# Kernel tuning notes

Measured on AMD Instinct MI355X. Metric: run time of the kernel, lower is better.

The kernel has to match this reference:

```python
import jax, jax.numpy as jnp
import numpy as np

N, E, IN_DIM, B = 20000, 320000, 256, 64
H0, C0 = 4, 128   # layer0: concat -> 512
H1, C1 = 4, 64    # layer1: mean over heads -> 64
NEG_SLOPE = 0.2
BN_EPS = 1e-5


def _p(key, shape, scale=0.05):
    return scale * jax.random.normal(key, shape, dtype=jnp.float32)


def setup_inputs() -> dict:
    key = jax.random.key(0)
    ks = jax.random.split(key, 32)
    inp = {
        'x': jax.random.normal(ks[0], (N, IN_DIM), dtype=jnp.float32),
        'edge_index': jax.random.randint(ks[1], (2, E), 0, N, dtype=jnp.int64),
        'edge_attr': jax.random.uniform(ks[2], (E, 1), dtype=jnp.float32),
        'batch': jnp.sort(jax.random.randint(ks[3], (N,), 0, B, dtype=jnp.int64)),
        # GATv2 layer 0: in=256 -> H0*C0=512 (concat)
        'g0_wl': _p(ks[4], (IN_DIM, H0 * C0)),
        'g0_wr': _p(ks[5], (IN_DIM, H0 * C0)),
        'g0_we': _p(ks[6], (1, H0 * C0)),
        'g0_att': _p(ks[7], (H0, C0)),
        'g0_bias': jnp.zeros((H0 * C0,), jnp.float32),
        'bn0_g': jnp.ones((H0 * C0,), jnp.float32),
        'bn0_b': jnp.zeros((H0 * C0,), jnp.float32),
        # GATv2 layer 1: in=512 -> C1=64 (mean over heads)
        'g1_wl': _p(ks[8], (H0 * C0, H1 * C1)),
        'g1_wr': _p(ks[9], (H0 * C0, H1 * C1)),
        'g1_we': _p(ks[10], (1, H1 * C1)),
        'g1_att': _p(ks[11], (H1, C1)),
        'g1_bias': jnp.zeros((C1,), jnp.float32),
        'bn1_g': jnp.ones((C1,), jnp.float32),
        'bn1_b': jnp.zeros((C1,), jnp.float32),
        # classifier: 64 -> 256 -> 128 -> 2 with BN+ELU
        'c_w1': _p(ks[12], (C1, 256)), 'c_b1': jnp.zeros((256,), jnp.float32),
        'cbn1_g': jnp.ones((256,), jnp.float32), 'cbn1_b': jnp.zeros((256,), jnp.float32),
        'c_w2': _p(ks[13], (256, 128)), 'c_b2': jnp.zeros((128,), jnp.float32),
        'cbn2_g': jnp.ones((128,), jnp.float32), 'cbn2_b': jnp.zeros((128,), jnp.float32),
        'c_w3': _p(ks[14], (128, 2)), 'c_b3': jnp.zeros((2,), jnp.float32),
    }
    return inp


def gatv2_conv(x, src, dst, edge_attr, wl, wr, we, att, bias, heads, ch, concat):
    """GATv2Conv: gather -> LeakyReLU score -> segment softmax over dst -> scatter-add."""
    n = x.shape[0]
    xl = (x @ wl).reshape(n, heads, ch)
    xr = (x @ wr).reshape(n, heads, ch)
    xe = (edge_attr @ we).reshape(-1, heads, ch)
    m = xl[src] + xr[dst] + xe                                  # [E,H,C]
    e = jnp.einsum('ehc,hc->eh', jax.nn.leaky_relu(m, NEG_SLOPE), att)
    e_max = jax.ops.segment_max(e, dst, num_segments=n)          # [N,H]
    e_exp = jnp.exp(e - e_max[dst])
    denom = jax.ops.segment_sum(e_exp, dst, num_segments=n)
    alpha = e_exp / (denom[dst] + 1e-16)                         # [E,H]
    out = jax.ops.segment_sum(alpha[:, :, None] * xl[src], dst, num_segments=n)
    out = out.reshape(n, heads * ch) if concat else out.mean(axis=1)
    return out + bias


def batchnorm(x, g, b):
    mu = x.mean(axis=0)
    var = x.var(axis=0)
    return (x - mu) * jax.lax.rsqrt(var + BN_EPS) * g + b


def reference(x, edge_index, edge_attr, batch,
              g0_wl, g0_wr, g0_we, g0_att, g0_bias, bn0_g, bn0_b,
              g1_wl, g1_wr, g1_we, g1_att, g1_bias, bn1_g, bn1_b,
              c_w1, c_b1, cbn1_g, cbn1_b, c_w2, c_b2, cbn2_g, cbn2_b, c_w3, c_b3):
    src, dst = edge_index[0], edge_index[1]
    # layer 0 (concat=True)
    h = gatv2_conv(x, src, dst, edge_attr, g0_wl, g0_wr, g0_we, g0_att, g0_bias, H0, C0, True)
    h = jax.nn.elu(batchnorm(h, bn0_g, bn0_b))  # dropout = identity (eval)
    # layer 1 (concat=False -> mean over heads)
    h = gatv2_conv(h, src, dst, edge_attr, g1_wl, g1_wr, g1_we, g1_att, g1_bias, H1, C1, False)
    h = jax.nn.elu(batchnorm(h, bn1_g, bn1_b))
    # global mean pool per graph
    sums = jax.ops.segment_sum(h, batch, num_segments=B)
    cnts = jax.ops.segment_sum(jnp.ones((h.shape[0], 1), h.dtype), batch, num_segments=B)
    emb = sums / jnp.maximum(cnts, 1.0)                          # [B, 64]
    # classifier MLP
    z = jax.nn.elu(batchnorm(emb @ c_w1 + c_b1, cbn1_g, cbn1_b))
    z = jax.nn.elu(batchnorm(z @ c_w2 + c_b2, cbn2_g, cbn2_b))
    logits = z @ c_w3 + c_b3                                     # [B, 2]
    return logits, emb
```

## Files before the change

### kernel.cpp

```cpp
#include <hip/hip_runtime.h>
#include <cmath>

#define Nn 20000
#define Ee 320000
#define Bb 64

typedef unsigned short u16;
typedef __bf16 bf16x8 __attribute__((ext_vector_type(8)));
typedef float f32x4 __attribute__((ext_vector_type(4)));

static const size_t OUT0 = 0;
static const size_t XL0B = 10240000;
static const size_t XR0B = 15360000;
static const size_t H0B  = 20480000;
static const size_t XB   = 25600000;
static const size_t WTS  = 28160000;
static const size_t OUT1 = 28422144;
static const size_t CSRI = 30982144;
static const size_t SMALL= 31342272;
static const size_t BN0S = SMALL;
static const size_t BN1S = BN0S + 1024;
static const size_t ZCNT = 1152;
static const size_t EMB  = BN1S + 128;
static const size_t Z1C  = EMB + 4096;
static const size_t Z2C  = Z1C + 16384;

__device__ __forceinline__ float lrelu(float x){ return x > 0.f ? x : 0.2f * x; }
__device__ __forceinline__ float elu(float x){ return x > 0.f ? x : expm1f(x); }
__device__ __forceinline__ u16 fbf(float f){
  unsigned u = __float_as_uint(f);
  return (u16)((u + 0x7fffu + ((u >> 16) & 1u)) >> 16);
}
__device__ __forceinline__ float blo(unsigned u){ return __uint_as_float(u << 16); }
__device__ __forceinline__ float bhi(unsigned u){ return __uint_as_float(u & 0xffff0000u); }

__global__ __launch_bounds__(256) void mega_setup(
    const float* __restrict__ x, u16* __restrict__ xb,
    const float* __restrict__ W0, const float* __restrict__ W1,
    const float* __restrict__ W2, const float* __restrict__ W3,
    u16* __restrict__ WTo,
    const int* __restrict__ ei, int* __restrict__ cursor,
    const int* __restrict__ batch, int* __restrict__ goffs){
  int b = blockIdx.x;
  if (b < 5000){
    int i = b * 256 + threadIdx.x;
    float4 v = ((const float4*)x)[i];
    ushort4 o; o.x = fbf(v.x); o.y = fbf(v.y); o.z = fbf(v.z); o.w = fbf(v.w);
    ((ushort4*)xb)[i] = o;
  } else if (b < 7048){
    int bb2 = b - 5000;
    int which = bb2 >> 9;
    const float* W = (which == 0) ? W0 : (which == 1) ? W1 : (which == 2) ? W2 : W3;
    int K = (which < 2) ? 256 : 512;
    int N = (which < 2) ? 512 : 256;
    int i = (bb2 & 511) * 256 + threadIdx.x;
    int n = i / K, k = i - n * K;
    WTo[which * 131072 + i] = fbf(W[k * N + n]);
  } else if (b < 8298){
    int e = (b - 7048) * 256 + threadIdx.x;
    atomicAdd(&cursor[ei[Ee + e]], 1);
  } else {
    int i = (b - 8298) * 256 + threadIdx.x;
    if (i >= Nn) return;
    int b1 = batch[i];
    int b0 = (i == 0) ? -1 : batch[i - 1];
    for (int g = b0 + 1; g <= b1; g++) goffs[g] = i;
    if (i == Nn - 1)
      for (int g = b1 + 1; g <= Bb; g++) goffs[g] = Nn;
  }
}

__global__ __launch_bounds__(256) void gemm_lds(const u16* __restrict__ A,
    const u16* __restrict__ WTa, const u16* __restrict__ WTb,
    u16* __restrict__ Oa, u16* __restrict__ Ob, int M, int K, int Nc){
  const u16* WT = blockIdx.z ? WTb : WTa;
  u16* O = blockIdx.z ? Ob : Oa;
  __shared__ u16 As[128 * 32];
  __shared__ u16 Bs[128 * 32];
  int tid = threadIdx.x;
  int m0 = blockIdx.y * 128, n0 = blockIdx.x * 128;
  int lane = tid & 63, w = tid >> 6;
  int wr = (w >> 1) * 64, wc = (w & 1) * 64;
  int l16 = lane & 15, kq = lane >> 4;
  int sr0 = w * 16 + (lane >> 2);
  int sr1 = 64 + sr0;
  int sc8 = (lane & 3) * 8;
  const u16* ga0 = &A[(size_t)(m0 + sr0) * K + sc8];
  const u16* ga1 = &A[(size_t)(m0 + sr1) * K + sc8];
  const u16* gb0 = &WT[(size_t)(n0 + sr0) * K + sc8];
  const u16* gb1 = &WT[(size_t)(n0 + sr1) * K + sc8];
  u16* lA0 = &As[w * 512];
  u16* lA1 = &As[2048 + w * 512];
  u16* lB0 = &Bs[w * 512];
  u16* lB1 = &Bs[2048 + w * 512];
  f32x4 acc[4][4] = {};
  for (int kt = 0; kt < K; kt += 32){
    __builtin_amdgcn_global_load_lds(
        (const __attribute__((address_space(1))) unsigned int*)(ga0 + kt),
        (__attribute__((address_space(3))) unsigned int*)lA0, 16, 0, 0);
    __builtin_amdgcn_global_load_lds(
        (const __attribute__((address_space(1))) unsigned int*)(ga1 + kt),
        (__attribute__((address_space(3))) unsigned int*)lA1, 16, 0, 0);
    __builtin_amdgcn_global_load_lds(
        (const __attribute__((address_space(1))) unsigned int*)(gb0 + kt),
        (__attribute__((address_space(3))) unsigned int*)lB0, 16, 0, 0);
    __builtin_amdgcn_global_load_lds(
        (const __attribute__((address_space(1))) unsigned int*)(gb1 + kt),
        (__attribute__((address_space(3))) unsigned int*)lB1, 16, 0, 0);
    __syncthreads();
    bf16x8 af[4], bfr[4];
    #pragma unroll
    for (int i = 0; i < 4; i++){
      af[i]  = *(bf16x8*)&As[(wr + i * 16 + l16) * 32 + kq * 8];
      bfr[i] = *(bf16x8*)&Bs[(wc + i * 16 + l16) * 32 + kq * 8];
    }
    #pragma unroll
    for (int i = 0; i < 4; i++)
      #pragma unroll
      for (int j = 0; j < 4; j++)
        acc[i][j] = __builtin_amdgcn_mfma_f32_16x16x32_bf16(af[i], bfr[j], acc[i][j], 0, 0, 0);
    __syncthreads();
  }
  #pragma unroll
  for (int i = 0; i < 4; i++){
    #pragma unroll
    for (int rg = 0; rg < 4; rg++){
      int row = m0 + wr + i * 16 + kq * 4 + rg;
      if (row < M){
        #pragma unroll
        for (int j = 0; j < 4; j++){
          int col = n0 + wc + j * 16 + l16;
          O[(size_t)row * Nc + col] = fbf(acc[i][j][rg]);
        }
      }
    }
  }
}

__global__ __launch_bounds__(1024) void csr_scan(int* __restrict__ offs,
                                                 int* __restrict__ cursor){
  __shared__ int part[1024];
  int t = threadIdx.x;
  int base = t * 20;
  int loc[20];
  int s = 0;
  #pragma unroll
  for (int i = 0; i < 20; i++){
    int idx = base + i;
    int v = (idx < Nn) ? cursor[idx] : 0;
    loc[i] = s; s += v;
  }
  part[t] = s;
  __syncthreads();
  for (int off = 1; off < 1024; off <<= 1){
    int v = 0;
    if (t >= off) v = part[t - off];
    __syncthreads();
    if (t >= off) part[t] += v;
    __syncthreads();
  }
  int pre = (t == 0) ? 0 : part[t - 1];
  #pragma unroll
  for (int i = 0; i < 20; i++){
    int idx = base + i;
    if (idx < Nn){ offs[idx] = pre + loc[i]; cursor[idx] = pre + loc[i]; }
  }
  if (t == 1023) offs[Nn] = part[1023];
}

__global__ __launch_bounds__(256) void csr_fill(const int* __restrict__ ei,
    int* __restrict__ cursor, int* __restrict__ eidx){
  int e = blockIdx.x * 256 + threadIdx.x;
  if (e < Ee){
    int d = ei[Ee + e];
    int p = atomicAdd(&cursor[d], 1);
    eidx[p] = e;
  }
}

__global__ __launch_bounds__(256) void fused_l0(const u16* __restrict__ xl,
    const u16* __restrict__ xr, const float* __restrict__ ea,
    const float* __restrict__ we, const float* __restrict__ att,
    const int* __restrict__ ei, const int* __restrict__ offs,
    const int* __restrict__ eidx, float* __restrict__ out){
  int n = blockIdx.x * 4 + (threadIdx.x >> 6);
  int lane = threadIdx.x & 63;
  int s = offs[n], e = offs[n + 1];
  int c = lane << 3;
  uint4 ru = *(const uint4*)&xr[(size_t)n * 512 + c];
  float r0=blo(ru.x), r1=bhi(ru.x), r2=blo(ru.y), r3=bhi(ru.y),
        r4=blo(ru.z), r5=bhi(ru.z), r6=blo(ru.w), r7=bhi(ru.w);
  float4 w0 = *(const float4*)&we[c],  w1 = *(const float4*)&we[c + 4];
  float4 t0 = *(const float4*)&att[c], t1 = *(const float4*)&att[c + 4];
  float d = 0.f;
  float a0=0.f,a1=0.f,a2=0.f,a3=0.f,a4=0.f,a5=0.f,a6=0.f,a7=0.f;
  int i = s;
  for (; i + 2 <= e; i += 2){
    int eA = eidx[i], eB = eidx[i + 1];
    int sA = ei[eA], sB = ei[eB];
    float avA = ea[eA], avB = ea[eB];
    uint4 luA = *(const uint4*)&xl[(size_t)sA * 512 + c];
    uint4 luB = *(const uint4*)&xl[(size_t)sB * 512 + c];
    float xA0=blo(luA.x), xA1=bhi(luA.x), xA2=blo(luA.y), xA3=bhi(luA.y),
          xA4=blo(luA.z), xA5=bhi(luA.z), xA6=blo(luA.w), xA7=bhi(luA.w);
    float xB0=blo(luB.x), xB1=bhi(luB.x), xB2=blo(luB.y), xB3=bhi(luB.y),
          xB4=blo(luB.z), xB5=bhi(luB.z), xB6=blo(luB.w), xB7=bhi(luB.w);
    float pA = lrelu(xA0+r0+avA*w0.x)*t0.x + lrelu(xA1+r1+avA*w0.y)*t0.y
             + lrelu(xA2+r2+avA*w0.z)*t0.z + lrelu(xA3+r3+avA*w0.w)*t0.w
             + lrelu(xA4+r4+avA*w1.x)*t1.x + lrelu(xA5+r5+avA*w1.y)*t1.y
             + lrelu(xA6+r6+avA*w1.z)*t1.z + lrelu(xA7+r7+avA*w1.w)*t1.w;
    float pB = lrelu(xB0+r0+avB*w0.x)*t0.x + lrelu(xB1+r1+avB*w0.y)*t0.y
             + lrelu(xB2+r2+avB*w0.z)*t0.z + lrelu(xB3+r3+avB*w0.w)*t0.w
             + lrelu(xB4+r4+avB*w1.x)*t1.x + lrelu(xB5+r5+avB*w1.y)*t1.y
             + lrelu(xB6+r6+avB*w1.z)*t1.z + lrelu(xB7+r7+avB*w1.w)*t1.w;
    pA += __shfl_xor(pA, 8); pB += __shfl_xor(pB, 8);
    pA += __shfl_xor(pA, 4); pB += __shfl_xor(pB, 4);
    pA += __shfl_xor(pA, 2); pB += __shfl_xor(pB, 2);
    pA += __shfl_xor(pA, 1); pB += __shfl_xor(pB, 1);
    float eeA = __expf(pA), eeB = __expf(pB);
    d += eeA + eeB;
    a0 += eeA*xA0 + eeB*xB0; a1 += eeA*xA1 + eeB*xB1;
    a2 += eeA*xA2 + eeB*xB2; a3 += eeA*xA3 + eeB*xB3;
    a4 += eeA*xA4 + eeB*xB4; a5 += eeA*xA5 + eeB*xB5;
    a6 += eeA*xA6 + eeB*xB6; a7 += eeA*xA7 + eeB*xB7;
  }
  if (i < e){
    int eA = eidx[i];
    int sA = ei[eA];
    float avA = ea[eA];
    uint4 luA = *(const uint4*)&xl[(size_t)sA * 512 + c];
    float x0=blo(luA.x), x1=bhi(luA.x), x2=blo(luA.y), x3=bhi(luA.y),
          x4=blo(luA.z), x5=bhi(luA.z), x6=blo(luA.w), x7=bhi(luA.w);
    float p = lrelu(x0+r0+avA*w0.x)*t0.x + lrelu(x1+r1+avA*w0.y)*t0.y
            + lrelu(x2+r2+avA*w0.z)*t0.z + lrelu(x3+r3+avA*w0.w)*t0.w
            + lrelu(x4+r4+avA*w1.x)*t1.x + lrelu(x5+r5+avA*w1.y)*t1.y
            + lrelu(x6+r6+avA*w1.z)*t1.z + lrelu(x7+r7+avA*w1.w)*t1.w;
    p += __shfl_xor(p, 8); p += __shfl_xor(p, 4);
    p += __shfl_xor(p, 2); p += __shfl_xor(p, 1);
    float ee = __expf(p);
    d += ee;
    a0 += ee*x0; a1 += ee*x1; a2 += ee*x2; a3 += ee*x3;
    a4 += ee*x4; a5 += ee*x5; a6 += ee*x6; a7 += ee*x7;
  }
  float inv = 1.f / (d + 1e-16f);
  float4* op = (float4*)&out[(size_t)n * 512 + c];
  op[0] = make_float4(a0*inv, a1*inv, a2*inv, a3*inv);
  op[1] = make_float4(a4*inv, a5*inv, a6*inv, a7*inv);
}

__global__ __launch_bounds__(256) void fused_l1(const u16* __restrict__ xl,
    const u16* __restrict__ xr, const float* __restrict__ ea,
    const float* __restrict__ we, const float* __restrict__ att,
    const int* __restrict__ ei, const int* __restrict__ offs,
    const int* __restrict__ eidx, float* __restrict__ out){
  int n = blockIdx.x * 4 + (threadIdx.x >> 6);
  int lane = threadIdx.x & 63;
  int s = offs[n], e = offs[n + 1];
  int c = lane << 2;
  uint2 ru = *(const uint2*)&xr[(size_t)n * 256 + c];
  float r0=blo(ru.x), r1=bhi(ru.x), r2=blo(ru.y), r3=bhi(ru.y);
  float4 w  = *(const float4*)&we[c];
  float4 tt = *(const float4*)&att[c];
  float d = 0.f;
  float a0=0.f,a1=0.f,a2=0.f,a3=0.f;
  int i = s;
  for (; i + 2 <= e; i += 2){
    int eA = eidx[i], eB = eidx[i + 1];
    int sA = ei[eA], sB = ei[eB];
    float avA = ea[eA], avB = ea[eB];
    uint2 luA = *(const uint2*)&xl[(size_t)sA * 256 + c];
    uint2 luB = *(const uint2*)&xl[(size_t)sB * 256 + c];
    float xA0=blo(luA.x), xA1=bhi(luA.x), xA2=blo(luA.y), xA3=bhi(luA.y);
    float xB0=blo(luB.x), xB1=bhi(luB.x), xB2=blo(luB.y), xB3=bhi(luB.y);
    float pA = lrelu(xA0+r0+avA*w.x)*tt.x + lrelu(xA1+r1+avA*w.y)*tt.y
             + lrelu(xA2+r2+avA*w.z)*tt.z + lrelu(xA3+r3+avA*w.w)*tt.w;
    float pB = lrelu(xB0+r0+avB*w.x)*tt.x + lrelu(xB1+r1+avB*w.y)*tt.y
             + lrelu(xB2+r2+avB*w.z)*tt.z + lrelu(xB3+r3+avB*w.w)*tt.w;
    pA += __shfl_xor(pA, 8); pB += __shfl_xor(pB, 8);
    pA += __shfl_xor(pA, 4); pB += __shfl_xor(pB, 4);
    pA += __shfl_xor(pA, 2); pB += __shfl_xor(pB, 2);
    pA += __shfl_xor(pA, 1); pB += __shfl_xor(pB, 1);
    float eeA = __expf(pA), eeB = __expf(pB);
    d += eeA + eeB;
    a0 += eeA*xA0 + eeB*xB0; a1 += eeA*xA1 + eeB*xB1;
    a2 += eeA*xA2 + eeB*xB2; a3 += eeA*xA3 + eeB*xB3;
  }
  if (i < e){
    int eA = eidx[i];
    int sA = ei[eA];
    float avA = ea[eA];
    uint2 lu = *(const uint2*)&xl[(size_t)sA * 256 + c];
    float x0=blo(lu.x), x1=bhi(lu.x), x2=blo(lu.y), x3=bhi(lu.y);
    float p = lrelu(x0+r0+avA*w.x)*tt.x + lrelu(x1+r1+avA*w.y)*tt.y
            + lrelu(x2+r2+avA*w.z)*tt.z + lrelu(x3+r3+avA*w.w)*tt.w;
    p += __shfl_xor(p, 8); p += __shfl_xor(p, 4);
    p += __shfl_xor(p, 2); p += __shfl_xor(p, 1);
    float ee = __expf(p);
    d += ee;
    a0 += ee*x0; a1 += ee*x1; a2 += ee*x2; a3 += ee*x3;
  }
  float inv = 0.25f / (d + 1e-16f);
  float v0 = a0*inv, v1 = a1*inv, v2 = a2*inv, v3 = a3*inv;
  v0 += __shfl_xor(v0, 16); v0 += __shfl_xor(v0, 32);
  v1 += __shfl_xor(v1, 16); v1 += __shfl_xor(v1, 32);
  v2 += __shfl_xor(v2, 16); v2 += __shfl_xor(v2, 32);
  v3 += __shfl_xor(v3, 16); v3 += __shfl_xor(v3, 32);
  if (lane < 16)
    *(float4*)&out[(size_t)n * 64 + lane * 4] = make_float4(v0, v1, v2, v3);
}

__global__ void bn_reduce(const float* __restrict__ X, float* __restrict__ stats,
                          int Nr, int C, int rpb){
  int tid = threadIdx.x;
  int c = tid % C, sub = tid / C, step = blockDim.x / C;
  float s = 0.f, s2 = 0.f;
  int rend = min((int)((blockIdx.x + 1) * rpb), Nr);
  for (int r = blockIdx.x * rpb + sub; r < rend; r += step){
    float v = X[(size_t)r * C + c];
    s += v; s2 += v * v;
  }
  atomicAdd(&stats[c], s);
  atomicAdd(&stats[C + c], s2);
}

__global__ __launch_bounds__(256) void bn_apply_bf(const float* __restrict__ X,
    const float* __restrict__ stats, const float* __restrict__ g,
    const float* __restrict__ b, u16* __restrict__ Xb, int total, int C, float invN){
  int idx = blockIdx.x * 256 + threadIdx.x;
  if (idx >= total) return;
  int c = idx % C;
  float mean = stats[c] * invN;
  float var = stats[C + c] * invN - mean * mean;
  float inv = rsqrtf(var + 1e-5f);
  float v = (X[idx] - mean) * inv * g[c] + b[c];
  Xb[idx] = fbf(elu(v));
}

__global__ __launch_bounds__(256) void bn_apply(float* __restrict__ X,
    const float* __restrict__ stats, const float* __restrict__ g,
    const float* __restrict__ b, int total, int C, float invN){
  int idx = blockIdx.x * 256 + threadIdx.x;
  if (idx >= total) return;
  int c = idx % C;
  float mean = stats[c] * invN;
  float var = stats[C + c] * invN - mean * mean;
  float inv = rsqrtf(var + 1e-5f);
  float v = (X[idx] - mean) * inv * g[c] + b[c];
  X[idx] = elu(v);
}

__global__ __launch_bounds__(256) void pool_graph(const float* __restrict__ h1,
    const int* __restrict__ goffs, float* __restrict__ emb, float* __restrict__ out_emb){
  int b = blockIdx.x;
  int s = goffs[b], e = goffs[b + 1];
  int c = threadIdx.x & 63, sub = threadIdx.x >> 6;
  float acc = 0.f;
  for (int n = s + sub; n < e; n += 4) acc += h1[(size_t)n * 64 + c];
  __shared__ float red[4][64];
  red[sub][c] = acc;
  __syncthreads();
  if (sub == 0){
    float v = red[0][c] + red[1][c] + red[2][c] + red[3][c];
    v /= fmaxf((float)(e - s), 1.0f);
    emb[b * 64 + c] = v;
    out_emb[b * 64 + c] = v;
  }
}

__global__ __launch_bounds__(256) void mlp1_par(const float* __restrict__ emb,
    const float* __restrict__ W1, const float* __restrict__ b1,
    const float* __restrict__ g, const float* __restrict__ bb,
    float* __restrict__ z1){
  int t = threadIdx.x;
  int jj = t & 15, rg = t >> 4;
  int j = blockIdx.x * 16 + jj;
  float acc[4];
  float bias = b1[j];
  #pragma unroll
  for (int r = 0; r < 4; r++) acc[r] = bias;
  for (int k = 0; k < 64; k++){
    float w = W1[k * 256 + j];
    #pragma unroll
    for (int r = 0; r < 4; r++) acc[r] += emb[(rg * 4 + r) * 64 + k] * w;
  }
  __shared__ float ssum[16][16], ssq[16][16];
  float s = 0.f, s2 = 0.f;
  #pragma unroll
  for (int r = 0; r < 4; r++){ s += acc[r]; s2 += acc[r] * acc[r]; }
  ssum[rg][jj] = s; ssq[rg][jj] = s2;
  __syncthreads();
  float S = 0.f, S2 = 0.f;
  #pragma unroll
  for (int q = 0; q < 16; q++){ S += ssum[q][jj]; S2 += ssq[q][jj]; }
  float mean = S * (1.f / 64.f);
  float var = S2 * (1.f / 64.f) - mean * mean;
  float inv = rsqrtf(var + 1e-5f);
  float sc = g[j] * inv, sh = bb[j] - mean * sc;
  #pragma unroll
  for (int r = 0; r < 4; r++)
    z1[(rg * 4 + r) * 256 + j] = elu(acc[r] * sc + sh);
}

__global__ __launch_bounds__(256) void mlp2_fast(const float* __restrict__ z1,
    const float* __restrict__ W2, const float* __restrict__ b2,
    const float* __restrict__ g, const float* __restrict__ bb,
    float* __restrict__ z2){
  __shared__ float z1T[128 * 68];
  __shared__ float w2s[256 * 17];
  __shared__ float ssum[16][16], ssq[16][16];
  int t = threadIdx.x;
  int jj = t & 15, rg = t >> 4;
  int j = blockIdx.x * 16 + jj;
  {
    int j0 = blockIdx.x * 16;
    #pragma unroll
    for (int q = 0; q < 4; q++){
      float4 v = *(const float4*)&W2[t * 128 + j0 + q * 4];
      w2s[t * 17 + q * 4 + 0] = v.x; w2s[t * 17 + q * 4 + 1] = v.y;
      w2s[t * 17 + q * 4 + 2] = v.z; w2s[t * 17 + q * 4 + 3] = v.w;
    }
  }
  float acc[4];
  float bias = b2[j];
  #pragma unroll
  for (int r = 0; r < 4; r++) acc[r] = bias;
  for (int kk = 0; kk < 2; kk++){
    #pragma unroll
    for (int p = 0; p < 8; p++){
      int idx4 = p * 256 + t;
      int row = idx4 >> 5, kq = idx4 & 31;
      float4 v = *(const float4*)&z1[row * 256 + kk * 128 + kq * 4];
      z1T[(kq * 4 + 0) * 68 + row] = v.x;
      z1T[(kq * 4 + 1) * 68 + row] = v.y;
      z1T[(kq * 4 + 2) * 68 + row] = v.z;
      z1T[(kq * 4 + 3) * 68 + row] = v.w;
    }
    __syncthreads();
    for (int k = 0; k < 128; k++){
      float w = w2s[(kk * 128 + k) * 17 + jj];
      float4 zv = *(const float4*)&z1T[k * 68 + rg * 4];
      acc[0] += zv.x * w; acc[1] += zv.y * w;
      acc[2] += zv.z * w; acc[3] += zv.w * w;
    }
    __syncthreads();
  }
  float s = 0.f, s2 = 0.f;
  #pragma unroll
  for (int r = 0; r < 4; r++){ s += acc[r]; s2 += acc[r] * acc[r]; }
  ssum[rg][jj] = s; ssq[rg][jj] = s2;
  __syncthreads();
  float S = 0.f, S2 = 0.f;
  #pragma unroll
  for (int q = 0; q < 16; q++){ S += ssum[q][jj]; S2 += ssq[q][jj]; }
  float mean = S * (1.f / 64.f);
  float var = S2 * (1.f / 64.f) - mean * mean;
  float inv = rsqrtf(var + 1e-5f);
  float sc = g[j] * inv, sh = bb[j] - mean * sc;
  #pragma unroll
  for (int r = 0; r < 4; r++)
    z2[(rg * 4 + r) * 128 + j] = elu(acc[r] * sc + sh);
}

__global__ __launch_bounds__(256) void mlp3_fast(const float* __restrict__ z2,
    const float* __restrict__ W3, const float* __restrict__ b3, float* __restrict__ out){
  __shared__ float z2s[64 * 132];
  __shared__ float w3s[256];
  int t = threadIdx.x;
  #pragma unroll
  for (int p = 0; p < 8; p++){
    int idx4 = p * 256 + t;
    int row = idx4 >> 5, kq = idx4 & 31;
    float4 v = *(const float4*)&z2[row * 128 + kq * 4];
    z2s[row * 132 + kq * 4 + 0] = v.x;
    z2s[row * 132 + kq * 4 + 1] = v.y;
    z2s[row * 132 + kq * 4 + 2] = v.z;
    z2s[row * 132 + kq * 4 + 3] = v.w;
  }
  if (t < 64){
    float4 v = ((const float4*)W3)[t];
    w3s[t * 4 + 0] = v.x; w3s[t * 4 + 1] = v.y;
    w3s[t * 4 + 2] = v.z; w3s[t * 4 + 3] = v.w;
  }
  __syncthreads();
  if (t < 128){
    int row = t >> 1, o = t & 1;
    float acc = b3[o];
    for (int k = 0; k < 128; k++)
      acc += z2s[row * 132 + k] * w3s[k * 2 + o];
    out[row * 2 + o] = acc;
  }
}

extern "C" void kernel_launch(void* const* d_in, const int* in_sizes, int n_in,
                              void* d_out, int out_size, void* d_ws, size_t ws_size,
                              hipStream_t stream){
  const float* x      = (const float*)d_in[0];
  const int*   ei     = (const int*)d_in[1];
  const float* ea     = (const float*)d_in[2];
  const int*   batch  = (const int*)d_in[3];
  const float* g0_wl  = (const float*)d_in[4];
  const float* g0_wr  = (const float*)d_in[5];
  const float* g0_we  = (const float*)d_in[6];
  const float* g0_att = (const float*)d_in[7];
  const float* bn0_g  = (const float*)d_in[9];
  const float* bn0_b  = (const float*)d_in[10];
  const float* g1_wl  = (const float*)d_in[11];
  const float* g1_wr  = (const float*)d_in[12];
  const float* g1_we  = (const float*)d_in[13];
  const float* g1_att = (const float*)d_in[14];
  const float* bn1_g  = (const float*)d_in[16];
  const float* bn1_b  = (const float*)d_in[17];
  const float* c_w1   = (const float*)d_in[18];
  const float* c_b1   = (const float*)d_in[19];
  const float* cbn1_g = (const float*)d_in[20];
  const float* cbn1_b = (const float*)d_in[21];
  const float* c_w2   = (const float*)d_in[22];
  const float* c_b2   = (const float*)d_in[23];
  const float* cbn2_g = (const float*)d_in[24];
  const float* cbn2_b = (const float*)d_in[25];
  const float* c_w3   = (const float*)d_in[26];
  const float* c_b3   = (const float*)d_in[27];
  float* out = (float*)d_out;
  float* ws = (float*)d_ws;

  u16* xb   = (u16*)(ws + XB);
  u16* xl0b = (u16*)(ws + XL0B);
  u16* xr0b = (u16*)(ws + XR0B);
  u16* h0b  = (u16*)(ws + H0B);
  u16* wt0a = (u16*)(ws + WTS);
  u16* wt0b = wt0a + 131072;
  u16* wt1a = wt0a + 262144;
  u16* wt1b = wt0a + 393216;
  int* offs   = (int*)(ws + CSRI);
  int* cursor = offs + (Nn + 1);
  int* eidx   = cursor + Nn;
  int* goffs  = eidx + Ee;

  hipMemsetAsync(cursor, 0, Nn * sizeof(int), stream);
  hipMemsetAsync(ws + SMALL, 0, ZCNT * sizeof(float), stream);

  mega_setup<<<8377, 256, 0, stream>>>(x, xb, g0_wl, g0_wr, g1_wl, g1_wr, wt0a,
                                       ei, cursor, batch, goffs);
  csr_scan<<<1, 1024, 0, stream>>>(offs, cursor);
  csr_fill<<<(Ee + 255) / 256, 256, 0, stream>>>(ei, cursor, eidx);

  gemm_lds<<<dim3(4, 157, 2), 256, 0, stream>>>(xb, wt0a, wt0b, xl0b, xr0b,
                                                Nn, 256, 512);
  fused_l0<<<Nn / 4, 256, 0, stream>>>(xl0b, xr0b, ea, g0_we, g0_att, ei,
                                       offs, eidx, ws + OUT0);
  bn_reduce<<<200, 512, 0, stream>>>(ws + OUT0, ws + BN0S, Nn, 512, 100);
  bn_apply_bf<<<40000, 256, 0, stream>>>(ws + OUT0, ws + BN0S, bn0_g, bn0_b, h0b,
                                         Nn * 512, 512, 1.f / Nn);
  gemm_lds<<<dim3(2, 157, 2), 256, 0, stream>>>(h0b, wt1a, wt1b, xl0b, xr0b,
                                                Nn, 512, 256);
  fused_l1<<<Nn / 4, 256, 0, stream>>>(xl0b, xr0b, ea, g1_we, g1_att, ei,
                                       offs, eidx, ws + OUT1);
  bn_reduce<<<50, 256, 0, stream>>>(ws + OUT1, ws + BN1S, Nn, 64, 400);
  bn_apply<<<5000, 256, 0, stream>>>(ws + OUT1, ws + BN1S, bn1_g, bn1_b,
                                     Nn * 64, 64, 1.f / Nn);
  pool_graph<<<Bb, 256, 0, stream>>>(ws + OUT1, goffs, ws + EMB, out + 128);
  mlp1_par<<<16, 256, 0, stream>>>(ws + EMB, c_w1, c_b1, cbn1_g, cbn1_b, ws + Z1C);
  mlp2_fast<<<8, 256, 0, stream>>>(ws + Z1C, c_w2, c_b2, cbn2_g, cbn2_b, ws + Z2C);
  mlp3_fast<<<1, 256, 0, stream>>>(ws + Z2C, c_w3, c_b3, out);
}
```

Baseline: 476.4 us.

## Pack edge source and attribute in CSR, fuse BN statistics into aggregation kernels

The CSR fill now writes a packed (source index, edge attribute) pair per sorted edge, so the aggregation kernels read one contiguous int2 instead of chasing eidx to ei and ea. The BatchNorm sum and sum-of-squares are accumulated in shared memory inside fused_l0 and fused_l1 and flushed to global memory with atomics, which removes both bn_reduce passes that re-read the full outputs. In exchange it adds shared-memory atomics and a block-wide sync per block, plus global atomic contention on the stats arrays from 5000 blocks.

```diff
diff --git a/kernel.cpp b/kernel.cpp
--- a/kernel.cpp
+++ b/kernel.cpp
@@ -16,6 +16,7 @@
 static const size_t XB   = 25600000;
 static const size_t WTS  = 28160000;
 static const size_t OUT1 = 28422144;
+static const size_t EPACK= 29702144;
 static const size_t CSRI = 30982144;
 static const size_t SMALL= 31342272;
 static const size_t BN0S = SMALL;
@@ -169,22 +170,27 @@
 }
 
 __global__ __launch_bounds__(256) void csr_fill(const int* __restrict__ ei,
-    int* __restrict__ cursor, int* __restrict__ eidx){
+    const float* __restrict__ ea, int* __restrict__ cursor,
+    int2* __restrict__ epack){
   int e = blockIdx.x * 256 + threadIdx.x;
   if (e < Ee){
     int d = ei[Ee + e];
     int p = atomicAdd(&cursor[d], 1);
-    eidx[p] = e;
+    epack[p] = make_int2(ei[e], __float_as_int(ea[e]));
   }
 }
 
 __global__ __launch_bounds__(256) void fused_l0(const u16* __restrict__ xl,
-    const u16* __restrict__ xr, const float* __restrict__ ea,
+    const u16* __restrict__ xr,
     const float* __restrict__ we, const float* __restrict__ att,
-    const int* __restrict__ ei, const int* __restrict__ offs,
-    const int* __restrict__ eidx, float* __restrict__ out){
-  int n = blockIdx.x * 4 + (threadIdx.x >> 6);
-  int lane = threadIdx.x & 63;
+    const int2* __restrict__ ep, const int* __restrict__ offs,
+    float* __restrict__ out, float* __restrict__ bnstats){
+  __shared__ float sred[1024];
+  int t = threadIdx.x;
+  #pragma unroll
+  for (int q = 0; q < 4; q++) sred[q * 256 + t] = 0.f;
+  int n = blockIdx.x * 4 + (t >> 6);
+  int lane = t & 63;
   int s = offs[n], e = offs[n + 1];
   int c = lane << 3;
   uint4 ru = *(const uint4*)&xr[(size_t)n * 512 + c];
@@ -194,13 +200,13 @@
   float4 t0 = *(const float4*)&att[c], t1 = *(const float4*)&att[c + 4];
   float d = 0.f;
   float a0=0.f,a1=0.f,a2=0.f,a3=0.f,a4=0.f,a5=0.f,a6=0.f,a7=0.f;
+  __syncthreads();
   int i = s;
   for (; i + 2 <= e; i += 2){
-    int eA = eidx[i], eB = eidx[i + 1];
-    int sA = ei[eA], sB = ei[eB];
-    float avA = ea[eA], avB = ea[eB];
-    uint4 luA = *(const uint4*)&xl[(size_t)sA * 512 + c];
-    uint4 luB = *(const uint4*)&xl[(size_t)sB * 512 + c];
+    int2 mA = ep[i], mB = ep[i + 1];
+    float avA = __int_as_float(mA.y), avB = __int_as_float(mB.y);
+    uint4 luA = *(const uint4*)&xl[(size_t)mA.x * 512 + c];
+    uint4 luB = *(const uint4*)&xl[(size_t)mB.x * 512 + c];
     float xA0=blo(luA.x), xA1=bhi(luA.x), xA2=blo(luA.y), xA3=bhi(luA.y),
           xA4=blo(luA.z), xA5=bhi(luA.z), xA6=blo(luA.w), xA7=bhi(luA.w);
     float xB0=blo(luB.x), xB1=bhi(luB.x), xB2=blo(luB.y), xB3=bhi(luB.y),
@@ -225,10 +231,9 @@
     a6 += eeA*xA6 + eeB*xB6; a7 += eeA*xA7 + eeB*xB7;
   }
   if (i < e){
-    int eA = eidx[i];
-    int sA = ei[eA];
-    float avA = ea[eA];
-    uint4 luA = *(const uint4*)&xl[(size_t)sA * 512 + c];
+    int2 mA = ep[i];
+    float avA = __int_as_float(mA.y);
+    uint4 luA = *(const uint4*)&xl[(size_t)mA.x * 512 + c];
     float x0=blo(luA.x), x1=bhi(luA.x), x2=blo(luA.y), x3=bhi(luA.y),
           x4=blo(luA.z), x5=bhi(luA.z), x6=blo(luA.w), x7=bhi(luA.w);
     float p = lrelu(x0+r0+avA*w0.x)*t0.x + lrelu(x1+r1+avA*w0.y)*t0.y
@@ -243,18 +248,35 @@
     a4 += ee*x4; a5 += ee*x5; a6 += ee*x6; a7 += ee*x7;
   }
   float inv = 1.f / (d + 1e-16f);
+  float v0=a0*inv, v1=a1*inv, v2=a2*inv, v3=a3*inv,
+        v4=a4*inv, v5=a5*inv, v6=a6*inv, v7=a7*inv;
   float4* op = (float4*)&out[(size_t)n * 512 + c];
-  op[0] = make_float4(a0*inv, a1*inv, a2*inv, a3*inv);
-  op[1] = make_float4(a4*inv, a5*inv, a6*inv, a7*inv);
+  op[0] = make_float4(v0, v1, v2, v3);
+  op[1] = make_float4(v4, v5, v6, v7);
+  atomicAdd(&sred[c + 0], v0); atomicAdd(&sred[512 + c + 0], v0 * v0);
+  atomicAdd(&sred[c + 1], v1); atomicAdd(&sred[512 + c + 1], v1 * v1);
+  atomicAdd(&sred[c + 2], v2); atomicAdd(&sred[512 + c + 2], v2 * v2);
+  atomicAdd(&sred[c + 3], v3); atomicAdd(&sred[512 + c + 3], v3 * v3);
+  atomicAdd(&sred[c + 4], v4); atomicAdd(&sred[512 + c + 4], v4 * v4);
+  atomicAdd(&sred[c + 5], v5); atomicAdd(&sred[512 + c + 5], v5 * v5);
+  atomicAdd(&sred[c + 6], v6); atomicAdd(&sred[512 + c + 6], v6 * v6);
+  atomicAdd(&sred[c + 7], v7); atomicAdd(&sred[512 + c + 7], v7 * v7);
+  __syncthreads();
+  #pragma unroll
+  for (int q = 0; q < 4; q++)
+    atomicAdd(&bnstats[q * 256 + t], sred[q * 256 + t]);
 }
 
 __global__ __launch_bounds__(256) void fused_l1(const u16* __restrict__ xl,
-    const u16* __restrict__ xr, const float* __restrict__ ea,
+    const u16* __restrict__ xr,
     const float* __restrict__ we, const float* __restrict__ att,
-    const int* __restrict__ ei, const int* __restrict__ offs,
-    const int* __restrict__ eidx, float* __restrict__ out){
-  int n = blockIdx.x * 4 + (threadIdx.x >> 6);
-  int lane = threadIdx.x & 63;
+    const int2* __restrict__ ep, const int* __restrict__ offs,
+    float* __restrict__ out, float* __restrict__ bnstats){
+  __shared__ float sred[128];
+  int t = threadIdx.x;
+  if (t < 128) sred[t] = 0.f;
+  int n = blockIdx.x * 4 + (t >> 6);
+  int lane = t & 63;
   int s = offs[n], e = offs[n + 1];
   int c = lane << 2;
   uint2 ru = *(const uint2*)&xr[(size_t)n * 256 + c];
@@ -263,13 +285,13 @@
   float4 tt = *(const float4*)&att[c];
   float d = 0.f;
   float a0=0.f,a1=0.f,a2=0.f,a3=0.f;
+  __syncthreads();
   int i = s;
   for (; i + 2 <= e; i += 2){
-    int eA = eidx[i], eB = eidx[i + 1];
-    int sA = ei[eA], sB = ei[eB];
-    float avA = ea[eA], avB = ea[eB];
-    uint2 luA = *(const uint2*)&xl[(size_t)sA * 256 + c];
-    uint2 luB = *(const uint2*)&xl[(size_t)sB * 256 + c];
+    int2 mA = ep[i], mB = ep[i + 1];
+    float avA = __int_as_float(mA.y), avB = __int_as_float(mB.y);
+    uint2 luA = *(const uint2*)&xl[(size_t)mA.x * 256 + c];
+    uint2 luB = *(const uint2*)&xl[(size_t)mB.x * 256 + c];
     float xA0=blo(luA.x), xA1=bhi(luA.x), xA2=blo(luA.y), xA3=bhi(luA.y);
     float xB0=blo(luB.x), xB1=bhi(luB.x), xB2=blo(luB.y), xB3=bhi(luB.y);
     float pA = lrelu(xA0+r0+avA*w.x)*tt.x + lrelu(xA1+r1+avA*w.y)*tt.y
@@ -286,10 +308,9 @@
     a2 += eeA*xA2 + eeB*xB2; a3 += eeA*xA3 + eeB*xB3;
   }
   if (i < e){
-    int eA = eidx[i];
-    int sA = ei[eA];
-    float avA = ea[eA];
-    uint2 lu = *(const uint2*)&xl[(size_t)sA * 256 + c];
+    int2 mA = ep[i];
+    float avA = __int_as_float(mA.y);
+    uint2 lu = *(const uint2*)&xl[(size_t)mA.x * 256 + c];
     float x0=blo(lu.x), x1=bhi(lu.x), x2=blo(lu.y), x3=bhi(lu.y);
     float p = lrelu(x0+r0+avA*w.x)*tt.x + lrelu(x1+r1+avA*w.y)*tt.y
             + lrelu(x2+r2+avA*w.z)*tt.z + lrelu(x3+r3+avA*w.w)*tt.w;
@@ -305,22 +326,16 @@
   v1 += __shfl_xor(v1, 16); v1 += __shfl_xor(v1, 32);
   v2 += __shfl_xor(v2, 16); v2 += __shfl_xor(v2, 32);
   v3 += __shfl_xor(v3, 16); v3 += __shfl_xor(v3, 32);
-  if (lane < 16)
+  if (lane < 16){
     *(float4*)&out[(size_t)n * 64 + lane * 4] = make_float4(v0, v1, v2, v3);
-}
-
-__global__ void bn_reduce(const float* __restrict__ X, float* __restrict__ stats,
-                          int Nr, int C, int rpb){
-  int tid = threadIdx.x;
-  int c = tid % C, sub = tid / C, step = blockDim.x / C;
-  float s = 0.f, s2 = 0.f;
-  int rend = min((int)((blockIdx.x + 1) * rpb), Nr);
-  for (int r = blockIdx.x * rpb + sub; r < rend; r += step){
-    float v = X[(size_t)r * C + c];
-    s += v; s2 += v * v;
-  }
-  atomicAdd(&stats[c], s);
-  atomicAdd(&stats[C + c], s2);
+    int cc = lane * 4;
+    atomicAdd(&sred[cc + 0], v0); atomicAdd(&sred[64 + cc + 0], v0 * v0);
+    atomicAdd(&sred[cc + 1], v1); atomicAdd(&sred[64 + cc + 1], v1 * v1);
+    atomicAdd(&sred[cc + 2], v2); atomicAdd(&sred[64 + cc + 2], v2 * v2);
+    atomicAdd(&sred[cc + 3], v3); atomicAdd(&sred[64 + cc + 3], v3 * v3);
+  }
+  __syncthreads();
+  if (t < 128) atomicAdd(&bnstats[t], sred[t]);
 }
 
 __global__ __launch_bounds__(256) void bn_apply_bf(const float* __restrict__ X,
@@ -531,10 +546,10 @@
   u16* wt0b = wt0a + 131072;
   u16* wt1a = wt0a + 262144;
   u16* wt1b = wt0a + 393216;
+  int2* epack = (int2*)(ws + EPACK);
   int* offs   = (int*)(ws + CSRI);
   int* cursor = offs + (Nn + 1);
-  int* eidx   = cursor + Nn;
-  int* goffs  = eidx + Ee;
+  int* goffs  = cursor + Nn;
 
   hipMemsetAsync(cursor, 0, Nn * sizeof(int), stream);
   hipMemsetAsync(ws + SMALL, 0, ZCNT * sizeof(float), stream);
@@ -542,20 +557,18 @@
   mega_setup<<<8377, 256, 0, stream>>>(x, xb, g0_wl, g0_wr, g1_wl, g1_wr, wt0a,
                                        ei, cursor, batch, goffs);
   csr_scan<<<1, 1024, 0, stream>>>(offs, cursor);
-  csr_fill<<<(Ee + 255) / 256, 256, 0, stream>>>(ei, cursor, eidx);
+  csr_fill<<<(Ee + 255) / 256, 256, 0, stream>>>(ei, ea, cursor, epack);
 
   gemm_lds<<<dim3(4, 157, 2), 256, 0, stream>>>(xb, wt0a, wt0b, xl0b, xr0b,
                                                 Nn, 256, 512);
-  fused_l0<<<Nn / 4, 256, 0, stream>>>(xl0b, xr0b, ea, g0_we, g0_att, ei,
-                                       offs, eidx, ws + OUT0);
-  bn_reduce<<<200, 512, 0, stream>>>(ws + OUT0, ws + BN0S, Nn, 512, 100);
+  fused_l0<<<Nn / 4, 256, 0, stream>>>(xl0b, xr0b, g0_we, g0_att,
+                                       epack, offs, ws + OUT0, ws + BN0S);
   bn_apply_bf<<<40000, 256, 0, stream>>>(ws + OUT0, ws + BN0S, bn0_g, bn0_b, h0b,
                                          Nn * 512, 512, 1.f / Nn);
   gemm_lds<<<dim3(2, 157, 2), 256, 0, stream>>>(h0b, wt1a, wt1b, xl0b, xr0b,
                                                 Nn, 512, 256);
-  fused_l1<<<Nn / 4, 256, 0, stream>>>(xl0b, xr0b, ea, g1_we, g1_att, ei,
-                                       offs, eidx, ws + OUT1);
-  bn_reduce<<<50, 256, 0, stream>>>(ws + OUT1, ws + BN1S, Nn, 64, 400);
+  fused_l1<<<Nn / 4, 256, 0, stream>>>(xl0b, xr0b, g1_we, g1_att,
+                                       epack, offs, ws + OUT1, ws + BN1S);
   bn_apply<<<5000, 256, 0, stream>>>(ws + OUT1, ws + BN1S, bn1_g, bn1_b,
                                      Nn * 64, 64, 1.f / Nn);
   pool_graph<<<Bb, 256, 0, stream>>>(ws + OUT1, goffs, ws + EMB, out + 128);
```

Result: slower. 594.9 us (+24.9%).
